# Kernel tuning notes

Hardware: AMD Instinct MI355X
Metric: run time of the kernel (lower is better)

The kernel has to match this reference:

```python
import jax, jax.numpy as jnp
import numpy as np

NX, NY, NT = 256, 256, 10          # N = [nx, ny, nt]
DX = DY = DZ = 20e-9               # dr (cell size, m)
DT = 5e-12                         # dt (s)
TIMESTEPS = 3000
F0 = 6.0e9                         # drive frequency (hard-coded in module)
MU0 = 4.0 * np.pi * 1e-7
CPW_XPOS = np.array([40, 48, 56, 64, 112, 120, 128, 136, 184, 192, 200, 208], dtype=np.int32)
CPW_ZPOS = 100e-9                  # scalar z offset of the CPW plane
NFIL = CPW_XPOS.shape[0]

_x = jnp.arange(NX, dtype=jnp.float32) * DX
_y = jnp.arange(NY, dtype=jnp.float32) * DY
XG, YG = jnp.meshgrid(_x, _y, indexing="ij")          # [nx, ny]
XFIL = _x[CPW_XPOS]                                    # [nfil]
DX2_FIL = (XG[None] - XFIL[:, None, None]) ** 2        # [nfil, nx, ny]


def setup_inputs() -> dict:
    key = jax.random.key(0)
    m = 0.02 * jax.random.normal(key, (NT, 3, NX, NY), dtype=jnp.float32)
    Msat = jnp.float32(8.0e5)      # saturation magnetization (A/m)
    return {"m": m, "Msat": Msat}


def _curl_y(Mx, Mz):
    # y-component of curl(M): dMx/dz - dMz/dx (numpy.gradient-style finite diffs)
    dMx_dz = jnp.gradient(Mx, axis=2) / DZ
    dMz_dx = jnp.gradient(Mz, axis=0) / DX
    return dMx_dz - dMz_dx         # [nx, ny, 2]


def _vector_potential_y(curl_y):
    # A_y at targets (i in cpw_xpos, all j) via Biot-Savart sum over the grid.
    # The distance does not depend on the duplicated z layer, so sum curl over z first.
    S = curl_y.sum(axis=2)                                      # [nx, ny]
    z2 = jnp.float32(CPW_ZPOS) ** 2

    def a_for_row(yj):                                          # one pickup y, all filaments
        dist = jnp.sqrt(DX2_FIL + (YG - yj)[None] ** 2 + z2)    # [nfil, nx, ny]
        frac = jnp.nan_to_num(S[None] / dist)
        return frac.sum(axis=(1, 2))                            # [nfil]

    a = jax.lax.map(a_for_row, _y)                              # [ny, nfil]
    return (MU0 / (4.0 * np.pi) * DX * DY * DZ) * a.T           # [nfil, ny]


def reference(m, Msat):
    def a_y_at(m_t):                                            # m_t: [3, nx, ny]
        M = m_t * Msat
        Mx = jnp.repeat(M[0][:, :, None], 2, axis=2)            # torch.cat((m_, m_), 2)
        Mz = jnp.repeat(M[2][:, :, None], 2, axis=2)
        return _vector_potential_y(_curl_y(Mx, Mz))

    A_all = jax.lax.map(a_y_at, m)                              # [nt, nfil, ny]
    # deltaV[t-1, f] = -sum_y(E_y) * dy with E_y = -(A_y - A_y_prev) / dt
    deltaV = (A_all[1:] - A_all[:-1]).sum(axis=2) * (DY / DT)   # [nt-1, nfil]

    t = jnp.arange(TIMESTEPS - NT + 1, TIMESTEPS, dtype=jnp.float32) * DT  # [nt-1]
    sin_vec = jnp.sin(2.0 * np.pi * F0 * t)
    cos_vec = jnp.cos(2.0 * np.pi * F0 * t)
    L = t.shape[0]
    norm = DT * F0 * 2.0 * np.pi / (np.pi * (L * DT * F0))      # == 2/L, kept literal
    re = jnp.sum(cos_vec[:, None] * deltaV, axis=0) * norm      # [nfil]
    im = jnp.sum(sin_vec[:, None] * deltaV, axis=0) * norm      # [nfil]
    ffit = cos_vec[:, None] * re[None, :] + sin_vec[:, None] * im[None, :]
    return deltaV, ffit
```

## Files before the change

kernel.cpp:

```cpp
#include <hip/hip_runtime.h>
#include <math.h>

#define GRID   65536
#define NFIL   12
#define NTm1   9
#define UMAX   216
#define GROUPS 64
#define RPG    4

static constexpr double PI_d = 3.14159265358979323846;

__constant__ int c_xpos[NFIL] = {40,48,56,64,112,120,128,136,184,192,200,208};

__global__ __launch_bounds__(256) void build_Ktab(float* __restrict__ Kt) {
    const int u = blockIdx.x;
    const int d = threadIdx.x;

    const double dxv = (double)u * 20e-9;
    const double r2  = dxv * dxv + 1e-14;
    const double dy  = (double)d * 20e-9;
    const double g   = 1.0 / sqrt(r2 + dy * dy);

    __shared__ double pref[256];
    pref[d] = g;
    __syncthreads();
    for (int off = 1; off < 256; off <<= 1) {
        const double add = (d >= off) ? pref[d - off] : 0.0;
        __syncthreads();
        pref[d] += add;
        __syncthreads();
    }
    const double g0 = 1.0 / sqrt(r2);
    Kt[(u << 8) + d] = (float)(pref[d] + pref[255 - d] - g0);
}

__global__ __launch_bounds__(256) void fused_dot(const float* __restrict__ m,
                                                 const float* __restrict__ Kt,
                                                 double* __restrict__ partials) {
    const int k = blockIdx.x / GROUPS;
    const int g = blockIdx.x % GROUPS;
    const int j = threadIdx.x;

    const float* mz0 = m + (size_t)(3 * k + 2) * GRID;
    const float* mz1 = m + (size_t)(3 * k + 5) * GRID;

    double acc[NFIL];
#pragma unroll
    for (int f = 0; f < NFIL; ++f) acc[f] = 0.0;

#pragma unroll
    for (int r = 0; r < RPG; ++r) {
        const int i  = g * RPG + r;
        const int im = (i == 0)   ? 0   : i - 1;
        const int ip = (i == 255) ? 255 : i + 1;
        const float sc = (i == 0 || i == 255) ? 1.0f : 0.5f;
        const float dm = sc * ((mz1[ip * 256 + j] - mz0[ip * 256 + j])
                             - (mz1[im * 256 + j] - mz0[im * 256 + j]));
        const double dmd = (double)dm;
#pragma unroll
        for (int f = 0; f < NFIL; ++f) {
            const int u = abs(i - c_xpos[f]);
            acc[f] = fma(dmd, (double)Kt[(u << 8) + j], acc[f]);
        }
    }

    __shared__ double lds[4][NFIL];
    const int lane = threadIdx.x & 63, wid = threadIdx.x >> 6;
#pragma unroll
    for (int f = 0; f < NFIL; ++f) {
        double v = acc[f];
        for (int off = 32; off > 0; off >>= 1)
            v += __shfl_down(v, off, 64);
        if (lane == 0) lds[wid][f] = v;
    }
    __syncthreads();
    if (threadIdx.x < NFIL)
        partials[(size_t)blockIdx.x * NFIL + threadIdx.x] =
            lds[0][threadIdx.x] + lds[1][threadIdx.x] +
            lds[2][threadIdx.x] + lds[3][threadIdx.x];
}

__global__ __launch_bounds__(128) void finalize(const double* __restrict__ partials,
                                                const float* __restrict__ msat_p,
                                                float* __restrict__ out) {
    __shared__ double cs[NTm1], sn[NTm1], re[NFIL], im[NFIL], dV[NTm1 * NFIL];
    const int t = threadIdx.x;
    if (t < NTm1) {
        const double tt = (double)(2991 + t) * 5e-12;
        const double ph = 2.0 * PI_d * 6.0e9 * tt;
        cs[t] = cos(ph);
        sn[t] = sin(ph);
    }
    if (t < NTm1 * NFIL) {
        const int k = t / NFIL, f = t - NFIL * k;
        double s = 0.0;
        for (int g = 0; g < GROUPS; ++g)
            s += partials[(size_t)(k * GROUPS + g) * NFIL + f];
        const double msat = (double)msat_p[0];
        const double coef = -2.0 * msat * 1e-7 * (20e-9) * (20e-9) * (20e-9) / 5e-12;
        dV[t] = coef * s;
    }
    __syncthreads();
    if (t < NFIL) {
        double r = 0.0, s = 0.0;
        for (int kk = 0; kk < NTm1; ++kk) {
            const double v = dV[kk * NFIL + t];
            r += cs[kk] * v;
            s += sn[kk] * v;
        }
        re[t] = r * (2.0 / 9.0);
        im[t] = s * (2.0 / 9.0);
    }
    __syncthreads();
    if (t < NTm1 * NFIL) {
        out[t] = (float)dV[t];
        const int kk = t / NFIL, f = t - NFIL * kk;
        out[NTm1 * NFIL + t] = (float)(cs[kk] * re[f] + sn[kk] * im[f]);
    }
}

extern "C" void kernel_launch(void* const* d_in, const int* in_sizes, int n_in,
                              void* d_out, int out_size, void* d_ws, size_t ws_size,
                              hipStream_t stream) {
    (void)in_sizes; (void)n_in; (void)out_size; (void)ws_size;
    const float* m      = (const float*)d_in[0];
    const float* msat_p = (const float*)d_in[1];
    float* out = (float*)d_out;

    float*  Kt       = (float*)d_ws;
    double* partials = (double*)((char*)d_ws + ((size_t)UMAX * 256 * sizeof(float) + 255 & ~(size_t)255));

    build_Ktab<<<UMAX, 256, 0, stream>>>(Kt);
    fused_dot <<<NTm1 * GROUPS, 256, 0, stream>>>(m, Kt, partials);
    finalize  <<<1, 128, 0, stream>>>(partials, msat_p, out);
}
```

Measured before the change: 67.23 us.

## Fuse finalize into dot kernel via last-block ticket; wave-level scan for kernel table

Removes the separate finalize launch. Each dot block takes an atomic ticket after writing its partials, and the last block to finish performs the final reduction and Fourier fit. The kernel-table builder now scans with per-lane register sums plus wavefront shuffles, replacing the shared-memory Hillis-Steele scan and its many barriers, and writes float4 results. The ticket counter is reset in the table kernel, which relies on stream ordering between the two launches.

```diff
diff --git a/kernel.cpp b/kernel.cpp
--- a/kernel.cpp
+++ b/kernel.cpp
@@ -1,42 +1,66 @@
 #include <hip/hip_runtime.h>
 #include <math.h>
 
-#define GRID   65536
-#define NFIL   12
-#define NTm1   9
-#define UMAX   216
-#define GROUPS 64
-#define RPG    4
+#define GRID    65536
+#define NFIL    12
+#define NTm1    9
+#define UMAX    216
+#define GROUPS  64
+#define RPG     4
+#define NBLK2   (NTm1 * GROUPS)
 
 static constexpr double PI_d = 3.14159265358979323846;
 
 __constant__ int c_xpos[NFIL] = {40,48,56,64,112,120,128,136,184,192,200,208};
 
-__global__ __launch_bounds__(256) void build_Ktab(float* __restrict__ Kt) {
-    const int u = blockIdx.x;
-    const int d = threadIdx.x;
+__global__ __launch_bounds__(256) void build_Ktab(float* __restrict__ Kt,
+                                                  unsigned* __restrict__ counter) {
+    if (blockIdx.x == 0 && threadIdx.x == 0) *counter = 0u;
+
+    const int u    = blockIdx.x * 4 + (threadIdx.x >> 6);
+    const int lane = threadIdx.x & 63;
+    if (u >= UMAX) return;
 
     const double dxv = (double)u * 20e-9;
     const double r2  = dxv * dxv + 1e-14;
-    const double dy  = (double)d * 20e-9;
-    const double g   = 1.0 / sqrt(r2 + dy * dy);
 
-    __shared__ double pref[256];
-    pref[d] = g;
-    __syncthreads();
-    for (int off = 1; off < 256; off <<= 1) {
-        const double add = (d >= off) ? pref[d - off] : 0.0;
-        __syncthreads();
-        pref[d] += add;
-        __syncthreads();
+    double g[4], P[4];
+#pragma unroll
+    for (int e = 0; e < 4; ++e) {
+        const double dy = (double)(4 * lane + e) * 20e-9;
+        g[e] = 1.0 / sqrt(r2 + dy * dy);
     }
+    P[0] = g[0]; P[1] = P[0] + g[1]; P[2] = P[1] + g[2]; P[3] = P[2] + g[3];
+
+    const double lsum = P[3];
+    double scan = lsum;
+#pragma unroll
+    for (int off = 1; off < 64; off <<= 1) {
+        const double v = __shfl_up(scan, off, 64);
+        if (lane >= off) scan += v;
+    }
+    const double excl = scan - lsum;
+#pragma unroll
+    for (int e = 0; e < 4; ++e) P[e] += excl;
+
+    double rev[4];
+#pragma unroll
+    for (int e = 0; e < 4; ++e)
+        rev[e] = __shfl(P[3 - e], 63 - lane, 64);
+
     const double g0 = 1.0 / sqrt(r2);
-    Kt[(u << 8) + d] = (float)(pref[d] + pref[255 - d] - g0);
+    float4 o;
+    o.x = (float)(P[0] + rev[0] - g0);
+    o.y = (float)(P[1] + rev[1] - g0);
+    o.z = (float)(P[2] + rev[2] - g0);
+    o.w = (float)(P[3] + rev[3] - g0);
+    *(float4*)(Kt + (u << 8) + 4 * lane) = o;
 }
 
-__global__ __launch_bounds__(256) void fused_dot(const float* __restrict__ m,
-                                                 const float* __restrict__ Kt,
-                                                 double* __restrict__ partials) {
+__global__ __launch_bounds__(256) void fused_dot_final(
+        const float* __restrict__ m, const float* __restrict__ Kt,
+        const float* __restrict__ msat_p, double* __restrict__ partials,
+        unsigned* __restrict__ counter, float* __restrict__ out) {
     const int k = blockIdx.x / GROUPS;
     const int g = blockIdx.x % GROUPS;
     const int j = threadIdx.x;
@@ -78,11 +102,15 @@
         partials[(size_t)blockIdx.x * NFIL + threadIdx.x] =
             lds[0][threadIdx.x] + lds[1][threadIdx.x] +
             lds[2][threadIdx.x] + lds[3][threadIdx.x];
-}
 
-__global__ __launch_bounds__(128) void finalize(const double* __restrict__ partials,
-                                                const float* __restrict__ msat_p,
-                                                float* __restrict__ out) {
+    __threadfence();
+    __shared__ unsigned s_tkt;
+    __syncthreads();
+    if (threadIdx.x == 0) s_tkt = atomicAdd(counter, 1u);
+    __syncthreads();
+    if (s_tkt != NBLK2 - 1) return;
+
+    __threadfence();
     __shared__ double cs[NTm1], sn[NTm1], re[NFIL], im[NFIL], dV[NTm1 * NFIL];
     const int t = threadIdx.x;
     if (t < NTm1) {
@@ -92,10 +120,10 @@
         sn[t] = sin(ph);
     }
     if (t < NTm1 * NFIL) {
-        const int k = t / NFIL, f = t - NFIL * k;
+        const int kk = t / NFIL, f = t - NFIL * kk;
         double s = 0.0;
-        for (int g = 0; g < GROUPS; ++g)
-            s += partials[(size_t)(k * GROUPS + g) * NFIL + f];
+        for (int gg = 0; gg < GROUPS; ++gg)
+            s += partials[(size_t)(kk * GROUPS + gg) * NFIL + f];
         const double msat = (double)msat_p[0];
         const double coef = -2.0 * msat * 1e-7 * (20e-9) * (20e-9) * (20e-9) / 5e-12;
         dV[t] = coef * s;
@@ -127,10 +155,12 @@
     const float* msat_p = (const float*)d_in[1];
     float* out = (float*)d_out;
 
-    float*  Kt       = (float*)d_ws;
-    double* partials = (double*)((char*)d_ws + ((size_t)UMAX * 256 * sizeof(float) + 255 & ~(size_t)255));
+    char* ws = (char*)d_ws;
+    float*    Kt       = (float*)ws;
+    size_t    off      = ((size_t)UMAX * 256 * sizeof(float) + 255) & ~(size_t)255;
+    double*   partials = (double*)(ws + off);
+    unsigned* counter  = (unsigned*)(ws + off + (size_t)NBLK2 * NFIL * sizeof(double));
 
-    build_Ktab<<<UMAX, 256, 0, stream>>>(Kt);
-    fused_dot <<<NTm1 * GROUPS, 256, 0, stream>>>(m, Kt, partials);
-    finalize  <<<1, 128, 0, stream>>>(partials, msat_p, out);
+    build_Ktab     <<<(UMAX + 3) / 4, 256, 0, stream>>>(Kt, counter);
+    fused_dot_final<<<NBLK2, 256, 0, stream>>>(m, Kt, msat_p, partials, counter, out);
 }
```

Measured after the change: 99.19 us. +47.5%, slower.
